# Kernel tuning notes

Hardware: AMD Instinct MI355X
Metric: run time of the kernel (lower is better)

Reference implementation:

```python
import jax, jax.numpy as jnp
import numpy as np


def setup_inputs() -> dict:
    key = jax.random.key(0)
    k1, k2 = jax.random.split(key)
    recon_points = jax.random.normal(k1, (4, 4096, 3), dtype=jnp.float32)
    gt_points = jax.random.normal(k2, (4, 4096, 3), dtype=jnp.float32)
    return {"recon_points": recon_points, "gt_points": gt_points}


def reference(recon_points, gt_points):
    # Pairwise squared distances: [B, N, M]
    diff = recon_points[:, :, None, :] - gt_points[:, None, :, :]  # [B,N,M,D]
    dist = jnp.sum(diff * diff, axis=3)                            # [B,N,M]
    dist_min1 = jnp.min(dist, axis=2)  # nearest gt for each recon point [B,N]
    dist_min2 = jnp.min(dist, axis=1)  # nearest recon for each gt point [B,M]
    loss = (jnp.mean(dist_min1) + jnp.mean(dist_min2)) / 2
    return loss
```

## Files before the change

kernel.cpp:

```cpp
#include <hip/hip_runtime.h>

#define CD_B 4
#define CD_N 4096
#define CD_TOTAL (CD_B * CD_N)
#define TILE 256

typedef float v2f __attribute__((ext_vector_type(2)));

__global__ __launch_bounds__(256, 4) void cd_tiles(const float* __restrict__ recon,
                                                   const float* __restrict__ gt,
                                                   float* __restrict__ pm,
                                                   float* __restrict__ out) {
    const int bid = blockIdx.x;
    const int b   = bid >> 8;
    const int ti  = (bid >> 4) & 15;
    const int tj  = bid & 15;
    const int t   = threadIdx.x;
    const int w   = t >> 6;
    const int l   = t & 63;

    if (bid == 0 && t == 0) out[0] = 0.f;

    __shared__ alignas(16) float rxs[TILE], rys[TILE], rzs[TILE], rns[TILE];
    __shared__ alignas(16) float gxs[TILE], gys[TILE], gzs[TILE], gns[TILE];
    __shared__ float part[4][TILE];

    {
        const float* rp = recon + ((size_t)(b * CD_N + ti * TILE) + t) * 3;
        const float* gp = gt    + ((size_t)(b * CD_N + tj * TILE) + t) * 3;
        const float rx = rp[0], ry = rp[1], rz = rp[2];
        const float gx = gp[0], gy = gp[1], gz = gp[2];
        rxs[t] = rx; rys[t] = ry; rzs[t] = rz;
        rns[t] = fmaf(rz, rz, fmaf(ry, ry, rx * rx));
        gxs[t] = gx; gys[t] = gy; gzs[t] = gz;
        gns[t] = fmaf(gz, gz, fmaf(gy, gy, gx * gx));
    }
    __syncthreads();

    const float INF = __builtin_inff();

    {
        const v2f a0x = -2.f * rxs[l],       a0y = -2.f * rys[l],       a0z = -2.f * rzs[l];
        const v2f a1x = -2.f * rxs[64 + l],  a1y = -2.f * rys[64 + l],  a1z = -2.f * rzs[64 + l];
        const v2f a2x = -2.f * rxs[128 + l], a2y = -2.f * rys[128 + l], a2z = -2.f * rzs[128 + l];
        const v2f a3x = -2.f * rxs[192 + l], a3y = -2.f * rys[192 + l], a3z = -2.f * rzs[192 + l];
        v2f m0 = INF, m1 = INF, m2 = INF, m3 = INF;
        const int jbase = w << 6;
        #pragma unroll 8
        for (int jj = 0; jj < 64; jj += 2) {
            const int j = jbase + jj;
            const v2f gx = *(const v2f*)&gxs[j];
            const v2f gy = *(const v2f*)&gys[j];
            const v2f gz = *(const v2f*)&gzs[j];
            const v2f gn = *(const v2f*)&gns[j];
            v2f d;
            d = __builtin_elementwise_fma(a0z, gz, gn);
            d = __builtin_elementwise_fma(a0y, gy, d);
            d = __builtin_elementwise_fma(a0x, gx, d);
            m0 = __builtin_elementwise_min(m0, d);
            d = __builtin_elementwise_fma(a1z, gz, gn);
            d = __builtin_elementwise_fma(a1y, gy, d);
            d = __builtin_elementwise_fma(a1x, gx, d);
            m1 = __builtin_elementwise_min(m1, d);
            d = __builtin_elementwise_fma(a2z, gz, gn);
            d = __builtin_elementwise_fma(a2y, gy, d);
            d = __builtin_elementwise_fma(a2x, gx, d);
            m2 = __builtin_elementwise_min(m2, d);
            d = __builtin_elementwise_fma(a3z, gz, gn);
            d = __builtin_elementwise_fma(a3y, gy, d);
            d = __builtin_elementwise_fma(a3x, gx, d);
            m3 = __builtin_elementwise_min(m3, d);
        }
        part[w][l]       = fminf(m0[0], m0[1]);
        part[w][64 + l]  = fminf(m1[0], m1[1]);
        part[w][128 + l] = fminf(m2[0], m2[1]);
        part[w][192 + l] = fminf(m3[0], m3[1]);
    }
    __syncthreads();
    {
        const float v = fminf(fminf(part[0][t], part[1][t]),
                              fminf(part[2][t], part[3][t]));
        const float dist = fmaxf(v + rns[t], 0.f);
        pm[(((b << 4) + ti) << 12) + (tj << 8) + t] = dist;
    }
    __syncthreads();

    {
        const v2f a0x = -2.f * gxs[l],       a0y = -2.f * gys[l],       a0z = -2.f * gzs[l];
        const v2f a1x = -2.f * gxs[64 + l],  a1y = -2.f * gys[64 + l],  a1z = -2.f * gzs[64 + l];
        const v2f a2x = -2.f * gxs[128 + l], a2y = -2.f * gys[128 + l], a2z = -2.f * gzs[128 + l];
        const v2f a3x = -2.f * gxs[192 + l], a3y = -2.f * gys[192 + l], a3z = -2.f * gzs[192 + l];
        v2f m0 = INF, m1 = INF, m2 = INF, m3 = INF;
        const int ibase = w << 6;
        #pragma unroll 8
        for (int ii = 0; ii < 64; ii += 2) {
            const int i = ibase + ii;
            const v2f rx = *(const v2f*)&rxs[i];
            const v2f ry = *(const v2f*)&rys[i];
            const v2f rz = *(const v2f*)&rzs[i];
            const v2f rn = *(const v2f*)&rns[i];
            v2f d;
            d = __builtin_elementwise_fma(a0z, rz, rn);
            d = __builtin_elementwise_fma(a0y, ry, d);
            d = __builtin_elementwise_fma(a0x, rx, d);
            m0 = __builtin_elementwise_min(m0, d);
            d = __builtin_elementwise_fma(a1z, rz, rn);
            d = __builtin_elementwise_fma(a1y, ry, d);
            d = __builtin_elementwise_fma(a1x, rx, d);
            m1 = __builtin_elementwise_min(m1, d);
            d = __builtin_elementwise_fma(a2z, rz, rn);
            d = __builtin_elementwise_fma(a2y, ry, d);
            d = __builtin_elementwise_fma(a2x, rx, d);
            m2 = __builtin_elementwise_min(m2, d);
            d = __builtin_elementwise_fma(a3z, rz, rn);
            d = __builtin_elementwise_fma(a3y, ry, d);
            d = __builtin_elementwise_fma(a3x, rx, d);
            m3 = __builtin_elementwise_min(m3, d);
        }
        part[w][l]       = fminf(m0[0], m0[1]);
        part[w][64 + l]  = fminf(m1[0], m1[1]);
        part[w][128 + l] = fminf(m2[0], m2[1]);
        part[w][192 + l] = fminf(m3[0], m3[1]);
    }
    __syncthreads();
    {
        const float v = fminf(fminf(part[0][t], part[1][t]),
                              fminf(part[2][t], part[3][t]));
        const float dist = fmaxf(v + gns[t], 0.f);
        pm[262144 + (((b << 4) + tj) << 12) + (ti << 8) + t] = dist;
    }
}

__global__ __launch_bounds__(256) void cd_gather(const float* __restrict__ pm,
                                                 float* __restrict__ out) {
    const int tid = blockIdx.x * 256 + threadIdx.x;
    const int p   = tid & 255;
    const int ot  = (tid >> 8) & 15;
    const int gb  = tid >> 12;
    const float* base = pm + ((((gb << 4) + ot) << 4) << 8) + p;

    float m = base[0];
    #pragma unroll
    for (int st = 1; st < 16; ++st) m = fminf(m, base[st << 8]);

    for (int off = 32; off; off >>= 1) m += __shfl_down(m, off);
    __shared__ float ws[4];
    const int t = threadIdx.x;
    if ((t & 63) == 0) ws[t >> 6] = m;
    __syncthreads();
    if (t == 0) {
        const float s = ws[0] + ws[1] + ws[2] + ws[3];
        atomicAdd(out, s * (0.5f / (float)CD_TOTAL));
    }
}

extern "C" void kernel_launch(void* const* d_in, const int* in_sizes, int n_in,
                              void* d_out, int out_size, void* d_ws, size_t ws_size,
                              hipStream_t stream) {
    const float* recon = (const float*)d_in[0];
    const float* gt    = (const float*)d_in[1];
    float* pm  = (float*)d_ws;
    float* out = (float*)d_out;

    cd_tiles<<<CD_B * 16 * 16, 256, 0, stream>>>(recon, gt, pm, out);
    cd_gather<<<128, 256, 0, stream>>>(pm, out);
}
```

Baseline: 69.55 us.

## Split each tile's two min directions into separate blocks and raise occupancy

Each block now handles only one direction of the nearest-neighbour search, and the grid doubles to 2048 blocks. Each block loads both point tiles but runs a single compute pass instead of two, and launch bounds ask for 8 blocks per CU instead of 4. The aim is more parallelism and occupancy with less serial work per block and fewer barriers. The cost is that both tiles are loaded from global memory twice overall.

```diff
diff --git a/kernel.cpp b/kernel.cpp
--- a/kernel.cpp
+++ b/kernel.cpp
@@ -7,68 +7,73 @@
 
 typedef float v2f __attribute__((ext_vector_type(2)));
 
-__global__ __launch_bounds__(256, 4) void cd_tiles(const float* __restrict__ recon,
+__global__ __launch_bounds__(256, 8) void cd_tiles(const float* __restrict__ recon,
                                                    const float* __restrict__ gt,
                                                    float* __restrict__ pm,
                                                    float* __restrict__ out) {
     const int bid = blockIdx.x;
-    const int b   = bid >> 8;
-    const int ti  = (bid >> 4) & 15;
-    const int tj  = bid & 15;
+    const int dir = bid >> 10;
+    const int rem = bid & 1023;
+    const int b   = rem >> 8;
+    const int ti  = (rem >> 4) & 15;
+    const int tj  = rem & 15;
     const int t   = threadIdx.x;
     const int w   = t >> 6;
     const int l   = t & 63;
 
     if (bid == 0 && t == 0) out[0] = 0.f;
 
-    __shared__ alignas(16) float rxs[TILE], rys[TILE], rzs[TILE], rns[TILE];
-    __shared__ alignas(16) float gxs[TILE], gys[TILE], gzs[TILE], gns[TILE];
+    const float* op = dir ? gt : recon;
+    const float* sp = dir ? recon : gt;
+
+    __shared__ alignas(16) float oxs[TILE], oys[TILE], ozs[TILE], ons[TILE];
+    __shared__ alignas(16) float sxs[TILE], sys[TILE], szs[TILE], sns[TILE];
     __shared__ float part[4][TILE];
 
     {
-        const float* rp = recon + ((size_t)(b * CD_N + ti * TILE) + t) * 3;
-        const float* gp = gt    + ((size_t)(b * CD_N + tj * TILE) + t) * 3;
-        const float rx = rp[0], ry = rp[1], rz = rp[2];
-        const float gx = gp[0], gy = gp[1], gz = gp[2];
-        rxs[t] = rx; rys[t] = ry; rzs[t] = rz;
-        rns[t] = fmaf(rz, rz, fmaf(ry, ry, rx * rx));
-        gxs[t] = gx; gys[t] = gy; gzs[t] = gz;
-        gns[t] = fmaf(gz, gz, fmaf(gy, gy, gx * gx));
+        const float* o = op + ((size_t)(b * CD_N + ti * TILE) + t) * 3;
+        const float* s = sp + ((size_t)(b * CD_N + tj * TILE) + t) * 3;
+        const float ox = o[0], oy = o[1], oz = o[2];
+        const float sx = s[0], sy = s[1], sz = s[2];
+        oxs[t] = ox; oys[t] = oy; ozs[t] = oz;
+        ons[t] = fmaf(oz, oz, fmaf(oy, oy, ox * ox));
+        sxs[t] = sx; sys[t] = sy; szs[t] = sz;
+        sns[t] = fmaf(sz, sz, fmaf(sy, sy, sx * sx));
     }
     __syncthreads();
 
     const float INF = __builtin_inff();
 
     {
-        const v2f a0x = -2.f * rxs[l],       a0y = -2.f * rys[l],       a0z = -2.f * rzs[l];
-        const v2f a1x = -2.f * rxs[64 + l],  a1y = -2.f * rys[64 + l],  a1z = -2.f * rzs[64 + l];
-        const v2f a2x = -2.f * rxs[128 + l], a2y = -2.f * rys[128 + l], a2z = -2.f * rzs[128 + l];
-        const v2f a3x = -2.f * rxs[192 + l], a3y = -2.f * rys[192 + l], a3z = -2.f * rzs[192 + l];
+        const v2f a0x = -2.f * oxs[l],       a0y = -2.f * oys[l],       a0z = -2.f * ozs[l];
+        const v2f a1x = -2.f * oxs[64 + l],  a1y = -2.f * oys[64 + l],  a1z = -2.f * ozs[64 + l];
+        const v2f a2x = -2.f * oxs[128 + l], a2y = -2.f * oys[128 + l], a2z = -2.f * ozs[128 + l];
+        const v2f a3x = -2.f * oxs[192 + l], a3y = -2.f * oys[192 + l], a3z = -2.f * ozs[192 + l];
         v2f m0 = INF, m1 = INF, m2 = INF, m3 = INF;
         const int jbase = w << 6;
         #pragma unroll 8
         for (int jj = 0; jj < 64; jj += 2) {
             const int j = jbase + jj;
-            const v2f gx = *(const v2f*)&gxs[j];
-            const v2f gy = *(const v2f*)&gys[j];
-            const v2f gz = *(const v2f*)&gzs[j];
-            const v2f gn = *(const v2f*)&gns[j];
+            const v2f sx = *(const v2f*)&sxs[j];
+            const v2f sy = *(const v2f*)&sys[j];
+            const v2f sz = *(const v2f*)&szs[j];
+            const v2f sn = *(const v2f*)&sns[j];
             v2f d;
-            d = __builtin_elementwise_fma(a0z, gz, gn);
-            d = __builtin_elementwise_fma(a0y, gy, d);
-            d = __builtin_elementwise_fma(a0x, gx, d);
+            d = __builtin_elementwise_fma(a0z, sz, sn);
+            d = __builtin_elementwise_fma(a0y, sy, d);
+            d = __builtin_elementwise_fma(a0x, sx, d);
             m0 = __builtin_elementwise_min(m0, d);
-            d = __builtin_elementwise_fma(a1z, gz, gn);
-            d = __builtin_elementwise_fma(a1y, gy, d);
-            d = __builtin_elementwise_fma(a1x, gx, d);
+            d = __builtin_elementwise_fma(a1z, sz, sn);
+            d = __builtin_elementwise_fma(a1y, sy, d);
+            d = __builtin_elementwise_fma(a1x, sx, d);
             m1 = __builtin_elementwise_min(m1, d);
-            d = __builtin_elementwise_fma(a2z, gz, gn);
-            d = __builtin_elementwise_fma(a2y, gy, d);
-            d = __builtin_elementwise_fma(a2x, gx, d);
+            d = __builtin_elementwise_fma(a2z, sz, sn);
+            d = __builtin_elementwise_fma(a2y, sy, d);
+            d = __builtin_elementwise_fma(a2x, sx, d);
             m2 = __builtin_elementwise_min(m2, d);
-            d = __builtin_elementwise_fma(a3z, gz, gn);
-            d = __builtin_elementwise_fma(a3y, gy, d);
-            d = __builtin_elementwise_fma(a3x, gx, d);
+            d = __builtin_elementwise_fma(a3z, sz, sn);
+            d = __builtin_elementwise_fma(a3y, sy, d);
+            d = __builtin_elementwise_fma(a3x, sx, d);
             m3 = __builtin_elementwise_min(m3, d);
         }
         part[w][l]       = fminf(m0[0], m0[1]);
@@ -80,54 +85,8 @@
     {
         const float v = fminf(fminf(part[0][t], part[1][t]),
                               fminf(part[2][t], part[3][t]));
-        const float dist = fmaxf(v + rns[t], 0.f);
-        pm[(((b << 4) + ti) << 12) + (tj << 8) + t] = dist;
-    }
-    __syncthreads();
-
-    {
-        const v2f a0x = -2.f * gxs[l],       a0y = -2.f * gys[l],       a0z = -2.f * gzs[l];
-        const v2f a1x = -2.f * gxs[64 + l],  a1y = -2.f * gys[64 + l],  a1z = -2.f * gzs[64 + l];
-        const v2f a2x = -2.f * gxs[128 + l], a2y = -2.f * gys[128 + l], a2z = -2.f * gzs[128 + l];
-        const v2f a3x = -2.f * gxs[192 + l], a3y = -2.f * gys[192 + l], a3z = -2.f * gzs[192 + l];
-        v2f m0 = INF, m1 = INF, m2 = INF, m3 = INF;
-        const int ibase = w << 6;
-        #pragma unroll 8
-        for (int ii = 0; ii < 64; ii += 2) {
-            const int i = ibase + ii;
-            const v2f rx = *(const v2f*)&rxs[i];
-            const v2f ry = *(const v2f*)&rys[i];
-            const v2f rz = *(const v2f*)&rzs[i];
-            const v2f rn = *(const v2f*)&rns[i];
-            v2f d;
-            d = __builtin_elementwise_fma(a0z, rz, rn);
-            d = __builtin_elementwise_fma(a0y, ry, d);
-            d = __builtin_elementwise_fma(a0x, rx, d);
-            m0 = __builtin_elementwise_min(m0, d);
-            d = __builtin_elementwise_fma(a1z, rz, rn);
-            d = __builtin_elementwise_fma(a1y, ry, d);
-            d = __builtin_elementwise_fma(a1x, rx, d);
-            m1 = __builtin_elementwise_min(m1, d);
-            d = __builtin_elementwise_fma(a2z, rz, rn);
-            d = __builtin_elementwise_fma(a2y, ry, d);
-            d = __builtin_elementwise_fma(a2x, rx, d);
-            m2 = __builtin_elementwise_min(m2, d);
-            d = __builtin_elementwise_fma(a3z, rz, rn);
-            d = __builtin_elementwise_fma(a3y, ry, d);
-            d = __builtin_elementwise_fma(a3x, rx, d);
-            m3 = __builtin_elementwise_min(m3, d);
-        }
-        part[w][l]       = fminf(m0[0], m0[1]);
-        part[w][64 + l]  = fminf(m1[0], m1[1]);
-        part[w][128 + l] = fminf(m2[0], m2[1]);
-        part[w][192 + l] = fminf(m3[0], m3[1]);
-    }
-    __syncthreads();
-    {
-        const float v = fminf(fminf(part[0][t], part[1][t]),
-                              fminf(part[2][t], part[3][t]));
-        const float dist = fmaxf(v + gns[t], 0.f);
-        pm[262144 + (((b << 4) + tj) << 12) + (ti << 8) + t] = dist;
+        const float dist = fmaxf(v + ons[t], 0.f);
+        pm[(dir << 18) + (((b << 4) + ti) << 12) + (tj << 8) + t] = dist;
     }
 }
 
@@ -162,6 +121,6 @@
     float* pm  = (float*)d_ws;
     float* out = (float*)d_out;
 
-    cd_tiles<<<CD_B * 16 * 16, 256, 0, stream>>>(recon, gt, pm, out);
+    cd_tiles<<<2 * CD_B * 16 * 16, 256, 0, stream>>>(recon, gt, pm, out);
     cd_gather<<<128, 256, 0, stream>>>(pm, out);
 }
```

After: 95.25 us. 1.37x slower.
